# Kernel optimization log

Measured on AMD Instinct MI355X. Metric: run time of the kernel, lower is better.

Reference implementation:

```python
import jax, jax.numpy as jnp
import numpy as np

N = 100000
E = 1600000
IN_C = 256
OUT_C = 128


def setup_inputs() -> dict:
    key = jax.random.key(0)
    ks = jax.random.split(key, 8)
    x = jax.random.normal(ks[0], (N, IN_C), dtype=jnp.float32)
    edge_index = jax.random.randint(ks[1], (2, E), 0, N, dtype=jnp.int64)
    # GCNConv params (weight + bias)
    W = jax.random.normal(ks[2], (IN_C, OUT_C), dtype=jnp.float32) / np.sqrt(IN_C)
    b = jnp.zeros((OUT_C,), dtype=jnp.float32)
    # residual Linear params
    Wr = jax.random.normal(ks[3], (IN_C, OUT_C), dtype=jnp.float32) / np.sqrt(IN_C)
    br = jnp.zeros((OUT_C,), dtype=jnp.float32)
    # LayerNorm params
    gamma = jnp.ones((OUT_C,), dtype=jnp.float32)
    beta = jnp.zeros((OUT_C,), dtype=jnp.float32)
    return {"x": x, "edge_index": edge_index, "W": W, "b": b,
            "Wr": Wr, "br": br, "gamma": gamma, "beta": beta}


def _gcn_conv(x, src, dst, W, b):
    # PyG GCNConv: add self-loops, symmetric degree normalization,
    # transform first (out < in), then gather-scale-scatter.
    n = x.shape[0]
    loops = jnp.arange(n, dtype=src.dtype)
    src = jnp.concatenate([src, loops])
    dst = jnp.concatenate([dst, loops])
    ones = jnp.ones_like(dst, dtype=x.dtype)
    deg = jax.ops.segment_sum(ones, dst, num_segments=n)  # [N]
    dinv = jnp.where(deg > 0, jax.lax.rsqrt(deg), 0.0)
    norm = dinv[src] * dinv[dst]                           # [E+N]
    h = x @ W                                              # [N, out]
    msg = h[src] * norm[:, None]                           # [E+N, out]
    agg = jax.ops.segment_sum(msg, dst, num_segments=n)    # [N, out]
    return agg + b


def _layer_norm(x, gamma, beta, eps=1e-5):
    mu = jnp.mean(x, axis=-1, keepdims=True)
    var = jnp.mean(jnp.square(x - mu), axis=-1, keepdims=True)
    return (x - mu) * jax.lax.rsqrt(var + eps) * gamma + beta


def reference(x, edge_index, W, b, Wr, br, gamma, beta):
    src, dst = edge_index[0], edge_index[1]
    res = x @ Wr + br
    h = _gcn_conv(x, src, dst, W, b)
    out = _layer_norm(h + res, gamma, beta)
    return jax.nn.relu(out)
```

## Files before the change

kernel.cpp:

```cpp
#include <hip/hip_runtime.h>

typedef __attribute__((ext_vector_type(8))) short bf16x8;
typedef __attribute__((ext_vector_type(4))) float f32x4;
typedef __attribute__((ext_vector_type(8))) unsigned short ushort8;
typedef __attribute__((ext_vector_type(4))) unsigned short ushort4v;

__device__ __forceinline__ unsigned short f2bf(float f) {
  unsigned int u = __float_as_uint(f);
  u = u + 0x7FFFu + ((u >> 16) & 1u);
  return (unsigned short)(u >> 16);
}
__device__ __forceinline__ float bflo(unsigned int u) { return __uint_as_float(u << 16); }
__device__ __forceinline__ float bfhi(unsigned int u) { return __uint_as_float(u & 0xFFFF0000u); }

#define GLOAD_LDS16(g, l)                                                            \
  __builtin_amdgcn_global_load_lds((const __attribute__((address_space(1))) void*)(g), \
                                   (__attribute__((address_space(3))) void*)(l), 16, 0, 0)

__global__ void k_prep_degrank(const float* __restrict__ W, const float* __restrict__ Wr,
                               unsigned short* __restrict__ Wb,
                               const int* __restrict__ dst, int* __restrict__ deg,
                               int* __restrict__ rank, int E) {
  if (blockIdx.x < 8) {
    int t = blockIdx.x * 256 + threadIdx.x;
    int col = t >> 3, g = t & 7;
    const float* Ws = (col < 128) ? (W + col) : (Wr + (col - 128));
#pragma unroll
    for (int kt = 0; kt < 4; ++kt) {
      ushort8 u;
#pragma unroll
      for (int j = 0; j < 8; ++j) u[j] = f2bf(Ws[(size_t)(kt * 64 + g * 8 + j) * 128]);
      *(ushort8*)&Wb[kt * 16384 + col * 64 + ((g ^ (col & 7)) * 8)] = u;
    }
    return;
  }
  int base = ((blockIdx.x - 8) * 256 + threadIdx.x) * 4;
  if (base + 3 < E) {
    int4 d = *(const int4*)(dst + base);
    int r0 = atomicAdd(&deg[d.x], 1);
    int r1 = atomicAdd(&deg[d.y], 1);
    int r2 = atomicAdd(&deg[d.z], 1);
    int r3 = atomicAdd(&deg[d.w], 1);
    *(int4*)(rank + base) = make_int4(r0, r1, r2, r3);
  } else {
    for (int e = base; e < E; ++e) rank[e] = atomicAdd(&deg[dst[e]], 1);
  }
}

__global__ void k_scanA(const int* __restrict__ deg, int* __restrict__ bsums, int N) {
  __shared__ int s[256];
  int t = threadIdx.x;
  int base = blockIdx.x * 1024 + t * 4;
  int ts = 0;
#pragma unroll
  for (int j = 0; j < 4; ++j) { int idx = base + j; ts += (idx < N) ? deg[idx] : 0; }
  s[t] = ts; __syncthreads();
  for (int off = 1; off < 256; off <<= 1) {
    int v = (t >= off) ? s[t - off] : 0;
    __syncthreads();
    s[t] += v;
    __syncthreads();
  }
  if (t == 255) bsums[blockIdx.x] = s[255];
}

__global__ void k_scanB(int* bsums, int nb) {
  __shared__ int s[128];
  int t = threadIdx.x;
  int v = (t < nb) ? bsums[t] : 0;
  s[t] = v; __syncthreads();
  for (int off = 1; off < 128; off <<= 1) {
    int a = (t >= off) ? s[t - off] : 0;
    __syncthreads();
    s[t] += a;
    __syncthreads();
  }
  if (t < nb) bsums[t] = s[t] - v;
}

__global__ void k_scanC_dinv(const int* __restrict__ deg, const int* __restrict__ bsums,
                             int* __restrict__ start, float* __restrict__ dinv, int N) {
  __shared__ int s[256];
  int t = threadIdx.x;
  int base = blockIdx.x * 1024 + t * 4;
  int v[4]; int ts = 0;
#pragma unroll
  for (int j = 0; j < 4; ++j) { int idx = base + j; v[j] = (idx < N) ? deg[idx] : 0; ts += v[j]; }
  s[t] = ts; __syncthreads();
  for (int off = 1; off < 256; off <<= 1) {
    int a = (t >= off) ? s[t - off] : 0;
    __syncthreads();
    s[t] += a;
    __syncthreads();
  }
  int run = bsums[blockIdx.x] + s[t] - ts;
#pragma unroll
  for (int j = 0; j < 4; ++j) {
    int idx = base + j;
    if (idx < N) {
      start[idx] = run;
      dinv[idx] = rsqrtf((float)(v[j] + 1));
    }
    run += v[j];
  }
}

__global__ __launch_bounds__(512) void k_gemm_fill(
    const float* __restrict__ x, const unsigned short* __restrict__ Wb,
    const float* __restrict__ br, const float* __restrict__ dinv,
    unsigned short* __restrict__ hs, float* res, int N,
    const int* __restrict__ src, const int* __restrict__ dst,
    const int* __restrict__ start, const int* __restrict__ rank,
    int* __restrict__ ssrc, int E)
{
  __shared__ unsigned short xt[128][72];
  __shared__ unsigned short wt[256 * 64];
  int tid = threadIdx.x;

  if (blockIdx.x & 1) {
    int base = ((blockIdx.x >> 1) * 512 + tid) * 4;
    if (base + 3 < E) {
      int4 d = *(const int4*)(dst + base);
      int4 r = *(const int4*)(rank + base);
      int4 s = *(const int4*)(src + base);
      ssrc[start[d.x] + r.x] = s.x;
      ssrc[start[d.y] + r.y] = s.y;
      ssrc[start[d.z] + r.z] = s.z;
      ssrc[start[d.w] + r.w] = s.w;
    } else {
      for (int e = base; e < E; ++e) ssrc[start[dst[e]] + rank[e]] = src[e];
    }
    return;
  }

  int lane = tid & 63, w = tid >> 6;
  int lo = lane & 15, hi = lane >> 4;
  int brow = (blockIdx.x >> 1) * 128;

  f32x4 acc[16];
#pragma unroll
  for (int c = 0; c < 16; ++c) acc[c] = (f32x4){0.f, 0.f, 0.f, 0.f};

  for (int kt = 0; kt < 4; ++kt) {
    int k0 = kt * 64;
    const unsigned short* gw = Wb + kt * 16384;
#pragma unroll
    for (int i = 0; i < 4; ++i) {
      int off = i * 4096 + tid * 8;
      GLOAD_LDS16(gw + off, &wt[off]);
    }
#pragma unroll
    for (int r = 0; r < 4; ++r) {
      int idx = tid + 512 * r;
      int row = idx >> 4, kq = idx & 15;
      int node = brow + row;
      float4 v = make_float4(0.f, 0.f, 0.f, 0.f);
      if (node < N) v = *(const float4*)(x + (size_t)node * 256 + k0 + kq * 4);
      ushort4v u;
      u[0] = f2bf(v.x); u[1] = f2bf(v.y); u[2] = f2bf(v.z); u[3] = f2bf(v.w);
      *(ushort4v*)(&xt[row][kq * 4]) = u;
    }
    __syncthreads();
#pragma unroll
    for (int kk = 0; kk < 2; ++kk) {
      bf16x8 a = *(const bf16x8*)(&xt[w * 16 + lo][kk * 32 + hi * 8]);
      int gsw = ((kk * 4 + hi) ^ (lo & 7)) * 8;
#pragma unroll
      for (int c = 0; c < 16; ++c) {
        bf16x8 b = *(const bf16x8*)(&wt[(c * 16 + lo) * 64 + gsw]);
        acc[c] = __builtin_amdgcn_mfma_f32_16x16x32_bf16(a, b, acc[c], 0, 0, 0);
      }
    }
    __syncthreads();
  }
#pragma unroll
  for (int c = 0; c < 16; ++c) {
    int colo = c * 16 + lo;
#pragma unroll
    for (int rg = 0; rg < 4; ++rg) {
      int row = brow + w * 16 + hi * 4 + rg;
      if (row < N) {
        float v = acc[c][rg];
        if (colo < 128) hs[(size_t)row * 128 + colo] = f2bf(v * dinv[row]);
        else            res[(size_t)row * 128 + (colo - 128)] = v + br[colo - 128];
      }
    }
  }
}

__global__ __launch_bounds__(256) void k_agg(
    const unsigned int* __restrict__ hsb, const float* resin,
    const float* __restrict__ dinv, const int* __restrict__ start,
    const int* __restrict__ deg, const int* __restrict__ ssrc,
    const float* __restrict__ bias, const float* __restrict__ gamma,
    const float* __restrict__ beta, float* out, int N)
{
  int node = blockIdx.x * 4 + (threadIdx.x >> 6);
  int lane = threadIdx.x & 63;
  if (node >= N) return;
  unsigned int su = hsb[(size_t)node * 64 + lane];
  float ax = bflo(su), ay = bfhi(su);
  int s0 = start[node], cnt = deg[node];
  const int* sp = ssrc + s0;
  int e = 0;
  for (; e + 8 <= cnt; e += 8) {
    int i0 = sp[e + 0], i1 = sp[e + 1], i2 = sp[e + 2], i3 = sp[e + 3];
    int i4 = sp[e + 4], i5 = sp[e + 5], i6 = sp[e + 6], i7 = sp[e + 7];
    unsigned int u0 = hsb[(size_t)i0 * 64 + lane];
    unsigned int u1 = hsb[(size_t)i1 * 64 + lane];
    unsigned int u2 = hsb[(size_t)i2 * 64 + lane];
    unsigned int u3 = hsb[(size_t)i3 * 64 + lane];
    unsigned int u4 = hsb[(size_t)i4 * 64 + lane];
    unsigned int u5 = hsb[(size_t)i5 * 64 + lane];
    unsigned int u6 = hsb[(size_t)i6 * 64 + lane];
    unsigned int u7 = hsb[(size_t)i7 * 64 + lane];
    float x01 = bflo(u0) + bflo(u1), x23 = bflo(u2) + bflo(u3);
    float x45 = bflo(u4) + bflo(u5), x67 = bflo(u6) + bflo(u7);
    float y01 = bfhi(u0) + bfhi(u1), y23 = bfhi(u2) + bfhi(u3);
    float y45 = bfhi(u4) + bfhi(u5), y67 = bfhi(u6) + bfhi(u7);
    ax += (x01 + x23) + (x45 + x67);
    ay += (y01 + y23) + (y45 + y67);
  }
  for (; e + 4 <= cnt; e += 4) {
    int i0 = sp[e + 0], i1 = sp[e + 1], i2 = sp[e + 2], i3 = sp[e + 3];
    unsigned int u0 = hsb[(size_t)i0 * 64 + lane];
    unsigned int u1 = hsb[(size_t)i1 * 64 + lane];
    unsigned int u2 = hsb[(size_t)i2 * 64 + lane];
    unsigned int u3 = hsb[(size_t)i3 * 64 + lane];
    ax += (bflo(u0) + bflo(u1)) + (bflo(u2) + bflo(u3));
    ay += (bfhi(u0) + bfhi(u1)) + (bfhi(u2) + bfhi(u3));
  }
  for (; e < cnt; ++e) {
    int s = sp[e];
    unsigned int u = hsb[(size_t)s * 64 + lane];
    ax += bflo(u); ay += bfhi(u);
  }
  float di = dinv[node];
  float2 r  = ((const float2*)resin)[(size_t)node * 64 + lane];
  float2 bb = ((const float2*)bias)[lane];
  float vx = ax * di + bb.x + r.x;
  float vy = ay * di + bb.y + r.y;
  float sum = vx + vy;
#pragma unroll
  for (int off = 32; off >= 1; off >>= 1) sum += __shfl_xor(sum, off, 64);
  float mean = sum * (1.0f / 128.0f);
  float dx = vx - mean, dy = vy - mean;
  float sq = dx * dx + dy * dy;
#pragma unroll
  for (int off = 32; off >= 1; off >>= 1) sq += __shfl_xor(sq, off, 64);
  float rstd = rsqrtf(sq * (1.0f / 128.0f) + 1e-5f);
  float2 g  = ((const float2*)gamma)[lane];
  float2 be = ((const float2*)beta)[lane];
  float ox = fmaxf(dx * rstd * g.x + be.x, 0.0f);
  float oy = fmaxf(dy * rstd * g.y + be.y, 0.0f);
  ((float2*)out)[(size_t)node * 64 + lane] = make_float2(ox, oy);
}

extern "C" void kernel_launch(void* const* d_in, const int* in_sizes, int n_in,
                              void* d_out, int out_size, void* d_ws, size_t ws_size,
                              hipStream_t stream) {
  const float* x     = (const float*)d_in[0];
  const int*   eidx  = (const int*)d_in[1];
  const float* W     = (const float*)d_in[2];
  const float* b     = (const float*)d_in[3];
  const float* Wr    = (const float*)d_in[4];
  const float* br    = (const float*)d_in[5];
  const float* gamma = (const float*)d_in[6];
  const float* beta  = (const float*)d_in[7];
  float* out = (float*)d_out;

  int N = in_sizes[0] / 256;
  int E = in_sizes[1] / 2;
  const int* srcI = eidx;
  const int* dstI = eidx + E;

  char* w = (char*)d_ws;
  size_t off = 0;
  auto alloc = [&](size_t bytes) -> void* {
    void* p = w + off;
    off += (bytes + 255) & ~(size_t)255;
    return p;
  };
  unsigned short* hs   = (unsigned short*)alloc((size_t)N * 128 * 2);
  int*   deg    = (int*)alloc((size_t)N * 4);
  float* dinv   = (float*)alloc((size_t)N * 4);
  int*   start  = (int*)alloc((size_t)N * 4);
  int*   rank   = (int*)alloc((size_t)E * 4);
  int*   ssrc   = (int*)alloc((size_t)E * 4);
  unsigned short* Wb = (unsigned short*)alloc((size_t)4 * 16384 * 2);
  int nb = (N + 1023) / 1024;
  int*   bsums  = (int*)alloc(((size_t)nb + 32) * 4);

  hipMemsetAsync(deg, 0, (size_t)N * 4, stream);
  int dgrid = (E / 4 + 255) / 256;
  k_prep_degrank<<<8 + dgrid, 256, 0, stream>>>(W, Wr, Wb, dstI, deg, rank, E);
  k_scanA<<<nb, 256, 0, stream>>>(deg, bsums, N);
  k_scanB<<<1, 128, 0, stream>>>(bsums, nb);
  k_scanC_dinv<<<nb, 256, 0, stream>>>(deg, bsums, start, dinv, N);
  int ggrid = (N + 127) / 128;
  k_gemm_fill<<<2 * ggrid, 512, 0, stream>>>(x, Wb, br, dinv, hs, out, N,
                                             srcI, dstI, start, rank, ssrc, E);
  k_agg  <<<(N + 3) / 4, 256, 0, stream>>>((const unsigned int*)hs, out, dinv, start, deg, ssrc,
                                           b, gamma, beta, out, N);
}
```

Before: 247.4 us.

## Co-schedule CSR fill warps inside GEMM blocks and swizzle x tile in LDS

Instead of launching separate blocks for the edge scatter (CSR fill) alongside GEMM blocks, each GEMM block gets two extra wavefronts that scatter a slice of edges per k-step, overlapping the scatter's memory traffic with MFMA work. The x tile in LDS drops its padding in favour of an XOR swizzle, saving LDS while avoiding bank conflicts. Fill wavefronts now take part in the block barriers, so slow scatters can stall the GEMM, and the larger block size may raise register pressure and lower occupancy.

```diff
diff --git a/kernel.cpp b/kernel.cpp
--- a/kernel.cpp
+++ b/kernel.cpp
@@ -105,7 +105,7 @@
   }
 }
 
-__global__ __launch_bounds__(512) void k_gemm_fill(
+__global__ __launch_bounds__(640) void k_gemm_fill(
     const float* __restrict__ x, const unsigned short* __restrict__ Wb,
     const float* __restrict__ br, const float* __restrict__ dinv,
     unsigned short* __restrict__ hs, float* res, int N,
@@ -113,66 +113,73 @@
     const int* __restrict__ start, const int* __restrict__ rank,
     int* __restrict__ ssrc, int E)
 {
-  __shared__ unsigned short xt[128][72];
+  __shared__ unsigned short xt[128 * 64];
   __shared__ unsigned short wt[256 * 64];
   int tid = threadIdx.x;
-
-  if (blockIdx.x & 1) {
-    int base = ((blockIdx.x >> 1) * 512 + tid) * 4;
-    if (base + 3 < E) {
-      int4 d = *(const int4*)(dst + base);
-      int4 r = *(const int4*)(rank + base);
-      int4 s = *(const int4*)(src + base);
-      ssrc[start[d.x] + r.x] = s.x;
-      ssrc[start[d.y] + r.y] = s.y;
-      ssrc[start[d.z] + r.z] = s.z;
-      ssrc[start[d.w] + r.w] = s.w;
+  bool isFill = tid >= 512;
+  int lane = tid & 63;
+  int lo = lane & 15, hi = lane >> 4;
+  int w = tid >> 6;
+  int brow = blockIdx.x * 128;
+  int ft = tid - 512;
+
+  f32x4 acc[16];
+#pragma unroll
+  for (int c = 0; c < 16; ++c) acc[c] = (f32x4){0.f, 0.f, 0.f, 0.f};
+
+  for (int kt = 0; kt < 4; ++kt) {
+    if (!isFill) {
+      int k0 = kt * 64;
+      const unsigned short* gw = Wb + kt * 16384;
+#pragma unroll
+      for (int i = 0; i < 4; ++i) {
+        int off = i * 4096 + tid * 8;
+        GLOAD_LDS16(gw + off, &wt[off]);
+      }
+#pragma unroll
+      for (int r = 0; r < 4; ++r) {
+        int idx = tid + 512 * r;
+        int row = idx >> 4, kq = idx & 15;
+        int node = brow + row;
+        float4 v = make_float4(0.f, 0.f, 0.f, 0.f);
+        if (node < N) v = *(const float4*)(x + (size_t)node * 256 + k0 + kq * 4);
+        ushort4v u;
+        u[0] = f2bf(v.x); u[1] = f2bf(v.y); u[2] = f2bf(v.z); u[3] = f2bf(v.w);
+        int g = kq >> 1, h = kq & 1;
+        *(ushort4v*)(&xt[row * 64 + ((g ^ (row & 7)) * 8) + h * 4]) = u;
+      }
     } else {
-      for (int e = base; e < E; ++e) ssrc[start[dst[e]] + rank[e]] = src[e];
-    }
-    return;
-  }
-
-  int lane = tid & 63, w = tid >> 6;
-  int lo = lane & 15, hi = lane >> 4;
-  int brow = (blockIdx.x >> 1) * 128;
-
-  f32x4 acc[16];
-#pragma unroll
-  for (int c = 0; c < 16; ++c) acc[c] = (f32x4){0.f, 0.f, 0.f, 0.f};
-
-  for (int kt = 0; kt < 4; ++kt) {
-    int k0 = kt * 64;
-    const unsigned short* gw = Wb + kt * 16384;
-#pragma unroll
-    for (int i = 0; i < 4; ++i) {
-      int off = i * 4096 + tid * 8;
-      GLOAD_LDS16(gw + off, &wt[off]);
-    }
-#pragma unroll
-    for (int r = 0; r < 4; ++r) {
-      int idx = tid + 512 * r;
-      int row = idx >> 4, kq = idx & 15;
-      int node = brow + row;
-      float4 v = make_float4(0.f, 0.f, 0.f, 0.f);
-      if (node < N) v = *(const float4*)(x + (size_t)node * 256 + k0 + kq * 4);
-      ushort4v u;
-      u[0] = f2bf(v.x); u[1] = f2bf(v.y); u[2] = f2bf(v.z); u[3] = f2bf(v.w);
-      *(ushort4v*)(&xt[row][kq * 4]) = u;
-    }
-    __syncthreads();
-#pragma unroll
-    for (int kk = 0; kk < 2; ++kk) {
-      bf16x8 a = *(const bf16x8*)(&xt[w * 16 + lo][kk * 32 + hi * 8]);
-      int gsw = ((kk * 4 + hi) ^ (lo & 7)) * 8;
-#pragma unroll
-      for (int c = 0; c < 16; ++c) {
-        bf16x8 b = *(const bf16x8*)(&wt[(c * 16 + lo) * 64 + gsw]);
-        acc[c] = __builtin_amdgcn_mfma_f32_16x16x32_bf16(a, b, acc[c], 0, 0, 0);
-      }
-    }
-    __syncthreads();
-  }
+      int base = ((blockIdx.x * 128 + ft) * 4 + kt) * 4;
+      if (base + 3 < E) {
+        int4 d = *(const int4*)(dst + base);
+        int4 r = *(const int4*)(rank + base);
+        int4 s = *(const int4*)(src + base);
+        ssrc[start[d.x] + r.x] = s.x;
+        ssrc[start[d.y] + r.y] = s.y;
+        ssrc[start[d.z] + r.z] = s.z;
+        ssrc[start[d.w] + r.w] = s.w;
+      } else {
+        for (int e = base; e < E && e < base + 4; ++e) ssrc[start[dst[e]] + rank[e]] = src[e];
+      }
+    }
+    __syncthreads();
+    if (!isFill) {
+#pragma unroll
+      for (int kk = 0; kk < 2; ++kk) {
+        int row = w * 16 + lo;
+        int gsel = kk * 4 + hi;
+        bf16x8 a = *(const bf16x8*)(&xt[row * 64 + ((gsel ^ (row & 7)) * 8)]);
+        int gsw = (gsel ^ (lo & 7)) * 8;
+#pragma unroll
+        for (int c = 0; c < 16; ++c) {
+          bf16x8 b = *(const bf16x8*)(&wt[(c * 16 + lo) * 64 + gsw]);
+          acc[c] = __builtin_amdgcn_mfma_f32_16x16x32_bf16(a, b, acc[c], 0, 0, 0);
+        }
+      }
+    }
+    __syncthreads();
+  }
+  if (isFill) return;
 #pragma unroll
   for (int c = 0; c < 16; ++c) {
     int colo = c * 16 + lo;
@@ -298,8 +305,8 @@
   k_scanB<<<1, 128, 0, stream>>>(bsums, nb);
   k_scanC_dinv<<<nb, 256, 0, stream>>>(deg, bsums, start, dinv, N);
   int ggrid = (N + 127) / 128;
-  k_gemm_fill<<<2 * ggrid, 512, 0, stream>>>(x, Wb, br, dinv, hs, out, N,
-                                             srcI, dstI, start, rank, ssrc, E);
+  k_gemm_fill<<<ggrid, 640, 0, stream>>>(x, Wb, br, dinv, hs, out, N,
+                                         srcI, dstI, start, rank, ssrc, E);
   k_agg  <<<(N + 3) / 4, 256, 0, stream>>>((const unsigned int*)hs, out, dinv, start, deg, ssrc,
                                            b, gamma, beta, out, N);
 }
```

Result: slower. 257.2 us (+4.0%).
